# Kernel tuning notes

Hardware: AMD Instinct MI355X
Metric: run time of the kernel (lower is better)

Reference implementation:

```python
import jax, jax.numpy as jnp
import numpy as np

B, N, D = 2, 2048, 1024
H, DH = 16, 64
DI = 4096
EPS = 1e-5
NEG_SLOPE = 0.01  # F.leaky_relu default


def _ln(x, g, b):
    mu = jnp.mean(x, axis=-1, keepdims=True)
    var = jnp.mean((x - mu) ** 2, axis=-1, keepdims=True)
    return (x - mu) * jax.lax.rsqrt(var + EPS) * g + b


def setup_inputs() -> dict:
    key = jax.random.key(0)
    ks = jax.random.split(key, 10)
    s = 0.02
    return {
        "Z": jax.random.normal(ks[0], (B, N, D), jnp.float32),
        "new_mask": jax.random.normal(ks[1], (B, N, N), jnp.float32),
        "mask": jax.random.uniform(ks[2], (B, N, N), jnp.float32),
        "ln1_g": jnp.ones((D,), jnp.float32),
        "ln1_b": jnp.zeros((D,), jnp.float32),
        "qkv_w": jax.random.normal(ks[3], (3 * D, D), jnp.float32) * s,
        "qkv_b": jnp.zeros((3 * D,), jnp.float32),
        "o_w": jax.random.normal(ks[4], (D, H * DH), jnp.float32) * s,
        "ln2_g": jnp.ones((D,), jnp.float32),
        "ln2_b": jnp.zeros((D,), jnp.float32),
        "p1_w": jax.random.normal(ks[5], (DI, D), jnp.float32) * s,
        "p1_b": jnp.zeros((DI,), jnp.float32),
        "p2_w": jax.random.normal(ks[6], (D, DI), jnp.float32) * s,
        "p2_b": jnp.zeros((D,), jnp.float32),
    }


def reference(Z, new_mask, mask, ln1_g, ln1_b, qkv_w, qkv_b, o_w, ln2_g, ln2_b, p1_w, p1_b, p2_w, p2_b):
    inp = Z
    Zn = _ln(Z, ln1_g, ln1_b)
    qkv = (Zn @ qkv_w.T + qkv_b).reshape(B, N, H, 3 * DH)
    # torch chunk order in the source: V, Q, K
    V, Q, K = jnp.split(qkv, 3, axis=3)  # each [B,N,H,DH]
    # scores: einsum('bnij,bmij->binm') == [B,H,N,N]
    W = jnp.einsum("bnhd,bmhd->bhnm", Q, K) / np.sqrt(DH) + new_mask[:, None]
    A = jax.nn.softmax(W, axis=3) * mask[:, None]
    attn = jnp.einsum("bhnm,bmhd->bnhd", A, V).reshape(B, N, D)
    attn = jnp.where(attn >= 0, attn, NEG_SLOPE * attn) @ o_w.T  # leaky_relu then o_net (no bias)
    Z1 = attn + inp
    Zn2 = _ln(Z1, ln2_g, ln2_b)
    h = jax.nn.relu(Zn2 @ p1_w.T + p1_b)
    return h @ p2_w.T + p2_b + Z1
```

## Files before the change

### kernel.cpp

```cpp
#include <hip/hip_runtime.h>

typedef unsigned short u16;
typedef __attribute__((ext_vector_type(8))) short bf16x8;
typedef __attribute__((ext_vector_type(4))) float f32x4;

#define DEV static __device__ __forceinline__

DEV u16 f2bf(float f) {
    unsigned u = __float_as_uint(f);
    u += 0x7FFFu + ((u >> 16) & 1u);
    return (u16)(u >> 16);
}

typedef const __attribute__((address_space(1))) void* gas1_t;
typedef __attribute__((address_space(3))) void* gas3_t;

DEV void gl_lds16(const u16* g, u16* l) {
    __builtin_amdgcn_global_load_lds((gas1_t)g, (gas3_t)l, 16, 0, 0);
}

DEV int sw8(int row, int chunk) { return row * 64 + ((chunk ^ (row & 7)) << 3); }

__global__ void cast_bf16(const float* __restrict__ in, u16* __restrict__ out, int n4) {
    int i = blockIdx.x * blockDim.x + threadIdx.x;
    if (i < n4) {
        float4 v = ((const float4*)in)[i];
        ushort4 o;
        o.x = f2bf(v.x); o.y = f2bf(v.y); o.z = f2bf(v.z); o.w = f2bf(v.w);
        ((ushort4*)out)[i] = o;
    }
}

__global__ void cast_qkv(const float* __restrict__ in, u16* __restrict__ out) {
    int i = blockIdx.x * 256 + threadIdx.x;
    int orow = i >> 8, cc = i & 255;
    int region = orow >> 10, rem = orow & 1023, h = rem >> 6, t = rem & 63;
    int srow = h * 192 + region * 64 + t;
    float4 v = ((const float4*)in)[srow * 256 + cc];
    ushort4 o;
    o.x = f2bf(v.x); o.y = f2bf(v.y); o.z = f2bf(v.z); o.w = f2bf(v.w);
    ((ushort4*)out)[i] = o;
}

__global__ void permute_bias(const float* __restrict__ in, float* __restrict__ out) {
    int i = blockIdx.x * 256 + threadIdx.x;
    if (i < 3072) {
        int region = i >> 10, rem = i & 1023, h = rem >> 6, t = rem & 63;
        out[i] = in[h * 192 + region * 64 + t];
    }
}

__global__ void pack_mask(const float* __restrict__ nm, const float* __restrict__ pm,
                          unsigned* __restrict__ out, int n4) {
    int i = blockIdx.x * blockDim.x + threadIdx.x;
    if (i < n4) {
        float4 a = ((const float4*)nm)[i];
        float4 b = ((const float4*)pm)[i];
        uint4 o;
        o.x = ((unsigned)f2bf(b.x) << 16) | f2bf(a.x * 1.4426950f);
        o.y = ((unsigned)f2bf(b.y) << 16) | f2bf(a.y * 1.4426950f);
        o.z = ((unsigned)f2bf(b.z) << 16) | f2bf(a.z * 1.4426950f);
        o.w = ((unsigned)f2bf(b.w) << 16) | f2bf(a.w * 1.4426950f);
        ((uint4*)out)[i] = o;
    }
}

__global__ __launch_bounds__(256) void ln_bf16(const float* __restrict__ x,
                                               const float* __restrict__ gam,
                                               const float* __restrict__ bet,
                                               u16* __restrict__ y) {
    const int row = blockIdx.x;
    const int t = threadIdx.x;
    const float4 v = ((const float4*)(x + (size_t)row * 1024))[t];
    float s = v.x + v.y + v.z + v.w;
    float ss = v.x * v.x + v.y * v.y + v.z * v.z + v.w * v.w;
#pragma unroll
    for (int o = 1; o < 64; o <<= 1) {
        s += __shfl_xor(s, o);
        ss += __shfl_xor(ss, o);
    }
    __shared__ float rs[4], rss[4];
    const int wave = t >> 6, lane = t & 63;
    if (lane == 0) { rs[wave] = s; rss[wave] = ss; }
    __syncthreads();
    const float tot = rs[0] + rs[1] + rs[2] + rs[3];
    const float totss = rss[0] + rss[1] + rss[2] + rss[3];
    const float mu = tot * (1.0f / 1024.0f);
    const float var = totss * (1.0f / 1024.0f) - mu * mu;
    const float rstd = rsqrtf(var + 1e-5f);
    const float4 g4 = ((const float4*)gam)[t];
    const float4 b4 = ((const float4*)bet)[t];
    ushort4 o;
    o.x = f2bf((v.x - mu) * rstd * g4.x + b4.x);
    o.y = f2bf((v.y - mu) * rstd * g4.y + b4.y);
    o.z = f2bf((v.z - mu) * rstd * g4.z + b4.z);
    o.w = f2bf((v.w - mu) * rstd * g4.w + b4.w);
    ((ushort4*)(y + (size_t)row * 1024))[t] = o;
}

template <int EPI>
__global__ __launch_bounds__(256, 2) void gemm_bt(const u16* __restrict__ A,
                                                  const u16* __restrict__ Bt,
                                                  const float* __restrict__ bias,
                                                  const float* __restrict__ res,
                                                  void* __restrict__ out0,
                                                  void* __restrict__ out1,
                                                  void* __restrict__ out2,
                                                  int M, int N, int K) {
    __shared__ __align__(16) u16 As[128 * 32];
    __shared__ __align__(16) u16 Bs[128 * 32];
    const int tid = threadIdx.x;
    const int wave = tid >> 6, lane = tid & 63;
    const int lhi = lane >> 4, llo = lane & 15;
    const int bx = blockIdx.x, by = blockIdx.y;

    const int arow = wave * 32 + (lane >> 2);
    const int acol = (lane & 3) * 8;
    const u16* gA = A + (size_t)(by * 128 + arow) * K + acol;
    const u16* gB = Bt + (size_t)(bx * 128 + arow) * K + acol;
    u16* lA = As + wave * 1024 + lane * 8;
    u16* lB = Bs + wave * 1024 + lane * 8;

    const int wr = wave >> 1, wc = wave & 1;
    const f32x4 zero = {0.f, 0.f, 0.f, 0.f};
    f32x4 acc[4][4];
#pragma unroll
    for (int i = 0; i < 4; i++)
#pragma unroll
        for (int j = 0; j < 4; j++) acc[i][j] = zero;

    for (int k0 = 0; k0 < K; k0 += 32) {
        __syncthreads();
        gl_lds16(gA, lA);
        gl_lds16(gA + 16 * (size_t)K, lA + 512);
        gl_lds16(gB, lB);
        gl_lds16(gB + 16 * (size_t)K, lB + 512);
        gA += 32; gB += 32;
        __syncthreads();
        bf16x8 af[4], bfr[4];
#pragma unroll
        for (int i = 0; i < 4; i++)
            af[i] = *(const bf16x8*)(As + (wr * 64 + i * 16 + llo) * 32 + lhi * 8);
#pragma unroll
        for (int j = 0; j < 4; j++)
            bfr[j] = *(const bf16x8*)(Bs + (wc * 64 + j * 16 + llo) * 32 + lhi * 8);
#pragma unroll
        for (int i = 0; i < 4; i++)
#pragma unroll
            for (int j = 0; j < 4; j++)
                acc[i][j] = __builtin_amdgcn_mfma_f32_16x16x32_bf16(af[i], bfr[j], acc[i][j], 0, 0, 0);
    }

    const int rbase = by * 128 + wr * 64 + lhi * 4;
    const int cbase = bx * 128 + wc * 64 + llo;
#pragma unroll
    for (int i = 0; i < 4; i++) {
#pragma unroll
        for (int j = 0; j < 4; j++) {
#pragma unroll
            for (int r = 0; r < 4; r++) {
                const int row = rbase + i * 16 + r;
                const int col = cbase + j * 16;
                float v = acc[i][j][r];
                if (EPI == 0) {
                    v += bias[col];
                    const int region = col >> 10;
                    const int c = col & 1023;
                    const int b = row >> 11, n = row & 2047;
                    if (region == 0) {
                        ((float*)out0)[(size_t)row * 1024 + c] = v;
                    } else {
                        const int h = c >> 6, t = c & 63;
                        u16* dst = (region == 1) ? (u16*)out1 : (u16*)out2;
                        dst[(((size_t)(b * 16 + h)) * 2048 + n) * 64 + t] = f2bf(v);
                    }
                } else if (EPI == 1) {
                    ((float*)out0)[(size_t)row * N + col] = v + res[(size_t)row * N + col];
                } else if (EPI == 2) {
                    v += bias[col];
                    v = v > 0.f ? v : 0.f;
                    ((u16*)out0)[(size_t)row * N + col] = f2bf(v);
                } else {
                    v += bias[col] + res[(size_t)row * N + col];
                    ((float*)out0)[(size_t)row * N + col] = v;
                }
            }
        }
    }
}

__global__ __launch_bounds__(256) void vtrans(const float* __restrict__ Vsc,
                                              u16* __restrict__ Vt) {
    __shared__ u16 Ts[64 * 72];
    const int nt = blockIdx.x;
    const int bh = blockIdx.y;
    const int b = bh >> 4, h = bh & 15;
    const int t = threadIdx.x;
    const int n0 = nt * 64;
    const int nr = t >> 2;
    const int dq = (t & 3) * 16;
    const float* src = Vsc + ((size_t)(b * 2048 + n0 + nr)) * 1024 + h * 64 + dq;
    float4 v0 = ((const float4*)src)[0];
    float4 v1 = ((const float4*)src)[1];
    float4 v2 = ((const float4*)src)[2];
    float4 v3 = ((const float4*)src)[3];
    u16* c0 = Ts + nr;
    c0[(dq + 0) * 72]  = f2bf(v0.x); c0[(dq + 1) * 72]  = f2bf(v0.y);
    c0[(dq + 2) * 72]  = f2bf(v0.z); c0[(dq + 3) * 72]  = f2bf(v0.w);
    c0[(dq + 4) * 72]  = f2bf(v1.x); c0[(dq + 5) * 72]  = f2bf(v1.y);
    c0[(dq + 6) * 72]  = f2bf(v1.z); c0[(dq + 7) * 72]  = f2bf(v1.w);
    c0[(dq + 8) * 72]  = f2bf(v2.x); c0[(dq + 9) * 72]  = f2bf(v2.y);
    c0[(dq + 10) * 72] = f2bf(v2.z); c0[(dq + 11) * 72] = f2bf(v2.w);
    c0[(dq + 12) * 72] = f2bf(v3.x); c0[(dq + 13) * 72] = f2bf(v3.y);
    c0[(dq + 14) * 72] = f2bf(v3.z); c0[(dq + 15) * 72] = f2bf(v3.w);
    __syncthreads();
    const int d = t >> 2, n8 = (t & 3) * 16;
    bf16x8 o0 = *(const bf16x8*)(Ts + d * 72 + n8);
    bf16x8 o1 = *(const bf16x8*)(Ts + d * 72 + n8 + 8);
    u16* dst = Vt + ((size_t)bh * 64 + d) * 2048 + n0 + n8;
    *(bf16x8*)dst = o0;
    *(bf16x8*)(dst + 8) = o1;
}

__global__ __launch_bounds__(256, 2) void attn_fused2(const u16* __restrict__ Qg,
                                                      const u16* __restrict__ Kg,
                                                      const u16* __restrict__ Vt,
                                                      const unsigned* __restrict__ Mp,
                                                      u16* __restrict__ attnL) {
    __shared__ __align__(16) u16 Qs[128 * 64];
    __shared__ __align__(16) u16 Ks[64 * 64];
    __shared__ __align__(16) u16 Vs[64 * 64];
    __shared__ __align__(16) u16 Ps[128 * 64];
    const int tid = threadIdx.x, wave = tid >> 6, lane = tid & 63;
    const int lhi = lane >> 4, llo = lane & 15;
    const int id = blockIdx.x;
    const int hh = id >> 5, bq = id & 31;
    const int b = bq >> 4, qt = bq & 15;
    const int bh = b * 16 + hh;
    const int q0 = qt * 128;
    const int l3 = lane >> 3, l7 = lane & 7;
    const int swcol = (l7 ^ (l3 & 7)) * 8;

#pragma unroll
    for (int s = 0; s < 4; s++) {
        const int row = wave * 32 + s * 8 + l3;
        gl_lds16(Qg + ((size_t)bh * 2048 + q0 + row) * 64 + swcol,
                 Qs + wave * 2048 + s * 512 + lane * 8);
    }

    const unsigned* Mpb = Mp + (size_t)b * 2048 * 2048;
    int midx[2][4];
#pragma unroll
    for (int i = 0; i < 2; i++)
#pragma unroll
        for (int r = 0; r < 4; r++)
            midx[i][r] = (q0 + wave * 32 + i * 16 + lhi * 4 + r) * 2048 + llo;

    const f32x4 zero = {0.f, 0.f, 0.f, 0.f};
    f32x4 accO[2][4];
    float lsum[2][4];
#pragma unroll
    for (int i = 0; i < 2; i++)
#pragma unroll
        for (int j = 0; j < 4; j++) accO[i][j] = zero;
#pragma unroll
    for (int i = 0; i < 2; i++)
#pragma unroll
        for (int r = 0; r < 4; r++) lsum[i][r] = 0.f;

    const float CS = 0.125f * 1.4426950f;

    for (int m0 = 0; m0 < 2048; m0 += 64) {
        __syncthreads();
#pragma unroll
        for (int s = 0; s < 2; s++) {
            const int row = wave * 16 + s * 8 + l3;
            gl_lds16(Kg + ((size_t)bh * 2048 + m0 + row) * 64 + swcol,
                     Ks + wave * 1024 + s * 512 + lane * 8);
            gl_lds16(Vt + ((size_t)bh * 64 + row) * 2048 + m0 + swcol,
                     Vs + wave * 1024 + s * 512 + lane * 8);
        }
        unsigned mv[2][4][4];
#pragma unroll
        for (int i = 0; i < 2; i++)
#pragma unroll
            for (int r = 0; r < 4; r++)
#pragma unroll
                for (int j = 0; j < 4; j++)
                    mv[i][r][j] = Mpb[midx[i][r] + m0 + j * 16];
        __syncthreads();

        f32x4 sacc[2][4];
#pragma unroll
        for (int i = 0; i < 2; i++)
#pragma unroll
            for (int j = 0; j < 4; j++) sacc[i][j] = zero;
#pragma unroll
        for (int kk = 0; kk < 2; kk++) {
            bf16x8 aq[2];
#pragma unroll
            for (int i = 0; i < 2; i++)
                aq[i] = *(const bf16x8*)(Qs + sw8(wave * 32 + i * 16 + llo, kk * 4 + lhi));
#pragma unroll
            for (int j = 0; j < 4; j++) {
                const bf16x8 bk = *(const bf16x8*)(Ks + sw8(j * 16 + llo, kk * 4 + lhi));
                sacc[0][j] = __builtin_amdgcn_mfma_f32_16x16x32_bf16(aq[0], bk, sacc[0][j], 0, 0, 0);
                sacc[1][j] = __builtin_amdgcn_mfma_f32_16x16x32_bf16(aq[1], bk, sacc[1][j], 0, 0, 0);
            }
        }

#pragma unroll
        for (int i = 0; i < 2; i++)
#pragma unroll
            for (int j = 0; j < 4; j++)
#pragma unroll
                for (int r = 0; r < 4; r++) {
                    const unsigned u = mv[i][r][j];
                    const float nm = __uint_as_float(u << 16);
                    const float pm = __uint_as_float(u & 0xFFFF0000u);
                    const float e = exp2f(fmaf(sacc[i][j][r], CS, nm));
                    lsum[i][r] += e;
                    const float p = e * pm;
                    const u16 pb = (u16)((__float_as_uint(p) + 0x8000u) >> 16);
                    const int q_rel = wave * 32 + i * 16 + lhi * 4 + r;
                    const int ch = (j * 2 + (llo >> 3)) ^ (q_rel & 7);
                    Ps[q_rel * 64 + ch * 8 + (llo & 7)] = pb;
                }

#pragma unroll
        for (int kk = 0; kk < 2; kk++) {
            bf16x8 ap[2];
#pragma unroll
            for (int i = 0; i < 2; i++)
                ap[i] = *(const bf16x8*)(Ps + sw8(wave * 32 + i * 16 + llo, kk * 4 + lhi));
#pragma unroll
            for (int jd = 0; jd < 4; jd++) {
                const bf16x8 bv = *(const bf16x8*)(Vs + sw8(jd * 16 + llo, kk * 4 + lhi));
                accO[0][jd] = __builtin_amdgcn_mfma_f32_16x16x32_bf16(ap[0], bv, accO[0][jd], 0, 0, 0);
                accO[1][jd] = __builtin_amdgcn_mfma_f32_16x16x32_bf16(ap[1], bv, accO[1][jd], 0, 0, 0);
            }
        }
    }

#pragma unroll
    for (int i = 0; i < 2; i++)
#pragma unroll
        for (int r = 0; r < 4; r++) {
#pragma unroll
            for (int o = 1; o < 16; o <<= 1) lsum[i][r] += __shfl_xor(lsum[i][r], o);
            lsum[i][r] = 1.0f / lsum[i][r];
        }
#pragma unroll
    for (int i = 0; i < 2; i++)
#pragma unroll
        for (int jd = 0; jd < 4; jd++)
#pragma unroll
            for (int r = 0; r < 4; r++) {
                float v = accO[i][jd][r] * lsum[i][r];
                v = v >= 0.f ? v : 0.01f * v;
                const int q = q0 + wave * 32 + i * 16 + lhi * 4 + r;
                attnL[((size_t)b * 2048 + q) * 1024 + hh * 64 + jd * 16 + llo] = f2bf(v);
            }
}

extern "C" void kernel_launch(void* const* d_in, const int* in_sizes, int n_in,
                              void* d_out, int out_size, void* d_ws, size_t ws_size,
                              hipStream_t stream) {
    const float* Z     = (const float*)d_in[0];
    const float* nmask = (const float*)d_in[1];
    const float* pmask = (const float*)d_in[2];
    const float* ln1_g = (const float*)d_in[3];
    const float* ln1_b = (const float*)d_in[4];
    const float* qkv_w = (const float*)d_in[5];
    const float* qkv_b = (const float*)d_in[6];
    const float* o_w   = (const float*)d_in[7];
    const float* ln2_g = (const float*)d_in[8];
    const float* ln2_b = (const float*)d_in[9];
    const float* p1_w  = (const float*)d_in[10];
    const float* p1_b  = (const float*)d_in[11];
    const float* p2_w  = (const float*)d_in[12];
    const float* p2_b  = (const float*)d_in[13];
    float* out = (float*)d_out;

    char* w = (char*)d_ws;
    auto take = [&](size_t bytes) -> char* {
        char* p = w;
        w += (bytes + 255) & ~(size_t)255;
        return p;
    };
    u16* qkvW   = (u16*)take((size_t)3072 * 1024 * 2);
    u16* oW     = (u16*)take((size_t)1024 * 1024 * 2);
    u16* p1W    = (u16*)take((size_t)4096 * 1024 * 2);
    u16* p2W    = (u16*)take((size_t)1024 * 4096 * 2);
    u16* Zn     = (u16*)take((size_t)4096 * 1024 * 2);
    u16* Qb     = (u16*)take((size_t)32 * 2048 * 64 * 2);
    u16* Kb     = (u16*)take((size_t)32 * 2048 * 64 * 2);
    u16* Vt     = (u16*)take((size_t)32 * 64 * 2048 * 2);
    u16* attnL  = (u16*)take((size_t)4096 * 1024 * 2);
    float* Z1   = (float*)take((size_t)4096 * 1024 * 4);
    u16* hbuf   = (u16*)take((size_t)4096 * 4096 * 2);
    unsigned* Mp = (unsigned*)take((size_t)2 * 2048 * 2048 * 4);
    float* pbias = (float*)take((size_t)3072 * 4);
    float* Vsc   = (float*)hbuf;

    cast_qkv<<<dim3(3072), 256, 0, stream>>>(qkv_w, qkvW);
    permute_bias<<<dim3(12), 256, 0, stream>>>(qkv_b, pbias);
    cast_bf16<<<dim3(1024), 256, 0, stream>>>(o_w, oW, 1024 * 1024 / 4);
    cast_bf16<<<dim3(4096), 256, 0, stream>>>(p1_w, p1W, 4096 * 1024 / 4);
    cast_bf16<<<dim3(4096), 256, 0, stream>>>(p2_w, p2W, 1024 * 4096 / 4);
    pack_mask<<<dim3(8192), 256, 0, stream>>>(nmask, pmask, Mp, 2 * 2048 * 2048 / 4);

    ln_bf16<<<dim3(4096), 256, 0, stream>>>(Z, ln1_g, ln1_b, Zn);
    gemm_bt<0><<<dim3(24, 32), 256, 0, stream>>>(Zn, qkvW, pbias, nullptr, Vsc, Qb, Kb, 4096, 3072, 1024);
    vtrans<<<dim3(32, 32), 256, 0, stream>>>(Vsc, Vt);
    attn_fused2<<<dim3(512), 256, 0, stream>>>(Qb, Kb, Vt, Mp, attnL);
    gemm_bt<1><<<dim3(8, 32), 256, 0, stream>>>(attnL, oW, nullptr, Z, Z1, nullptr, nullptr, 4096, 1024, 1024);
    ln_bf16<<<dim3(4096), 256, 0, stream>>>(Z1, ln2_g, ln2_b, Zn);
    gemm_bt<2><<<dim3(32, 32), 256, 0, stream>>>(Zn, p1W, p1_b, nullptr, hbuf, nullptr, nullptr, 4096, 4096, 1024);
    gemm_bt<3><<<dim3(8, 32), 256, 0, stream>>>(hbuf, p2W, p2_b, Z1, out, nullptr, nullptr, 4096, 1024, 4096);
}
```

Before: 476.3 us.

## Split-K narrow GEMMs with fused combine kernels and halve attention query tile

The two N=1024 GEMMs (o-proj and FFN down) now run with split-K=2 over a z grid dimension. They write fp32 partials into the reused mask buffer, and new combine kernels reduce the partials, with residual and bias folded in. LN2 is fused into the o-proj combine. The attention kernel now uses 64-row query tiles with 4 blocks per CU instead of 128-row tiles at 2 per CU, doubling the block count and using a padded P buffer. The aim is better occupancy and CU fill for grids that were too small (256 blocks, 512 blocks), at the cost of extra partial-sum traffic and less Q reuse per K/V tile.

```diff
diff --git a/kernel.cpp b/kernel.cpp
--- a/kernel.cpp
+++ b/kernel.cpp
@@ -98,26 +98,84 @@
     ((ushort4*)(y + (size_t)row * 1024))[t] = o;
 }
 
+__global__ __launch_bounds__(256) void ln2_comb(const float* __restrict__ p0,
+                                                const float* __restrict__ p1,
+                                                const float* __restrict__ Z,
+                                                const float* __restrict__ gam,
+                                                const float* __restrict__ bet,
+                                                float* __restrict__ Z1,
+                                                u16* __restrict__ y) {
+    const int row = blockIdx.x;
+    const int t = threadIdx.x;
+    const float4 a = ((const float4*)(p0 + (size_t)row * 1024))[t];
+    const float4 c = ((const float4*)(p1 + (size_t)row * 1024))[t];
+    const float4 z = ((const float4*)(Z + (size_t)row * 1024))[t];
+    float4 v;
+    v.x = a.x + c.x + z.x; v.y = a.y + c.y + z.y;
+    v.z = a.z + c.z + z.z; v.w = a.w + c.w + z.w;
+    ((float4*)(Z1 + (size_t)row * 1024))[t] = v;
+    float s = v.x + v.y + v.z + v.w;
+    float ss = v.x * v.x + v.y * v.y + v.z * v.z + v.w * v.w;
+#pragma unroll
+    for (int o = 1; o < 64; o <<= 1) {
+        s += __shfl_xor(s, o);
+        ss += __shfl_xor(ss, o);
+    }
+    __shared__ float rs[4], rss[4];
+    const int wave = t >> 6, lane = t & 63;
+    if (lane == 0) { rs[wave] = s; rss[wave] = ss; }
+    __syncthreads();
+    const float tot = rs[0] + rs[1] + rs[2] + rs[3];
+    const float totss = rss[0] + rss[1] + rss[2] + rss[3];
+    const float mu = tot * (1.0f / 1024.0f);
+    const float var = totss * (1.0f / 1024.0f) - mu * mu;
+    const float rstd = rsqrtf(var + 1e-5f);
+    const float4 g4 = ((const float4*)gam)[t];
+    const float4 b4 = ((const float4*)bet)[t];
+    ushort4 o;
+    o.x = f2bf((v.x - mu) * rstd * g4.x + b4.x);
+    o.y = f2bf((v.y - mu) * rstd * g4.y + b4.y);
+    o.z = f2bf((v.z - mu) * rstd * g4.z + b4.z);
+    o.w = f2bf((v.w - mu) * rstd * g4.w + b4.w);
+    ((ushort4*)(y + (size_t)row * 1024))[t] = o;
+}
+
+__global__ __launch_bounds__(256) void out_comb(const float* __restrict__ p0,
+                                                const float* __restrict__ p1,
+                                                const float* __restrict__ bias,
+                                                const float* __restrict__ Z1,
+                                                float* __restrict__ out) {
+    int i = blockIdx.x * 256 + threadIdx.x;
+    float4 a = ((const float4*)p0)[i];
+    float4 c = ((const float4*)p1)[i];
+    float4 z = ((const float4*)Z1)[i];
+    float4 b = ((const float4*)bias)[i & 255];
+    float4 o;
+    o.x = a.x + c.x + z.x + b.x; o.y = a.y + c.y + z.y + b.y;
+    o.z = a.z + c.z + z.z + b.z; o.w = a.w + c.w + z.w + b.w;
+    ((float4*)out)[i] = o;
+}
+
 template <int EPI>
 __global__ __launch_bounds__(256, 2) void gemm_bt(const u16* __restrict__ A,
                                                   const u16* __restrict__ Bt,
                                                   const float* __restrict__ bias,
-                                                  const float* __restrict__ res,
                                                   void* __restrict__ out0,
                                                   void* __restrict__ out1,
                                                   void* __restrict__ out2,
-                                                  int M, int N, int K) {
+                                                  int M, int N, int K, int ldk) {
     __shared__ __align__(16) u16 As[128 * 32];
     __shared__ __align__(16) u16 Bs[128 * 32];
     const int tid = threadIdx.x;
     const int wave = tid >> 6, lane = tid & 63;
     const int lhi = lane >> 4, llo = lane & 15;
     const int bx = blockIdx.x, by = blockIdx.y;
+    const int kz = blockIdx.z * K;
 
     const int arow = wave * 32 + (lane >> 2);
     const int acol = (lane & 3) * 8;
-    const u16* gA = A + (size_t)(by * 128 + arow) * K + acol;
-    const u16* gB = Bt + (size_t)(bx * 128 + arow) * K + acol;
+    const u16* gA = A + (size_t)(by * 128 + arow) * ldk + kz + acol;
+    const u16* gB = Bt + (size_t)(bx * 128 + arow) * ldk + kz + acol;
     u16* lA = As + wave * 1024 + lane * 8;
     u16* lB = Bs + wave * 1024 + lane * 8;
 
@@ -132,9 +190,9 @@
     for (int k0 = 0; k0 < K; k0 += 32) {
         __syncthreads();
         gl_lds16(gA, lA);
-        gl_lds16(gA + 16 * (size_t)K, lA + 512);
+        gl_lds16(gA + 16 * (size_t)ldk, lA + 512);
         gl_lds16(gB, lB);
-        gl_lds16(gB + 16 * (size_t)K, lB + 512);
+        gl_lds16(gB + 16 * (size_t)ldk, lB + 512);
         gA += 32; gB += 32;
         __syncthreads();
         bf16x8 af[4], bfr[4];
@@ -153,6 +211,7 @@
 
     const int rbase = by * 128 + wr * 64 + lhi * 4;
     const int cbase = bx * 128 + wc * 64 + llo;
+    float* pout = (EPI == 4) ? ((float*)out0 + (size_t)blockIdx.z * M * N) : (float*)out0;
 #pragma unroll
     for (int i = 0; i < 4; i++) {
 #pragma unroll
@@ -162,7 +221,7 @@
                 const int row = rbase + i * 16 + r;
                 const int col = cbase + j * 16;
                 float v = acc[i][j][r];
-                if (EPI == 0) {
+                if constexpr (EPI == 0) {
                     v += bias[col];
                     const int region = col >> 10;
                     const int c = col & 1023;
@@ -174,15 +233,12 @@
                         u16* dst = (region == 1) ? (u16*)out1 : (u16*)out2;
                         dst[(((size_t)(b * 16 + h)) * 2048 + n) * 64 + t] = f2bf(v);
                     }
-                } else if (EPI == 1) {
-                    ((float*)out0)[(size_t)row * N + col] = v + res[(size_t)row * N + col];
-                } else if (EPI == 2) {
+                } else if constexpr (EPI == 2) {
                     v += bias[col];
                     v = v > 0.f ? v : 0.f;
                     ((u16*)out0)[(size_t)row * N + col] = f2bf(v);
                 } else {
-                    v += bias[col] + res[(size_t)row * N + col];
-                    ((float*)out0)[(size_t)row * N + col] = v;
+                    pout[(size_t)row * N + col] = v;
                 }
             }
         }
@@ -222,53 +278,48 @@
     *(bf16x8*)(dst + 8) = o1;
 }
 
-__global__ __launch_bounds__(256, 2) void attn_fused2(const u16* __restrict__ Qg,
+__global__ __launch_bounds__(256, 4) void attn_fused4(const u16* __restrict__ Qg,
                                                       const u16* __restrict__ Kg,
                                                       const u16* __restrict__ Vt,
                                                       const unsigned* __restrict__ Mp,
                                                       u16* __restrict__ attnL) {
-    __shared__ __align__(16) u16 Qs[128 * 64];
+    __shared__ __align__(16) u16 Qs[64 * 64];
     __shared__ __align__(16) u16 Ks[64 * 64];
     __shared__ __align__(16) u16 Vs[64 * 64];
-    __shared__ __align__(16) u16 Ps[128 * 64];
+    __shared__ __align__(16) u16 Ps[64 * 72];
     const int tid = threadIdx.x, wave = tid >> 6, lane = tid & 63;
     const int lhi = lane >> 4, llo = lane & 15;
     const int id = blockIdx.x;
-    const int hh = id >> 5, bq = id & 31;
-    const int b = bq >> 4, qt = bq & 15;
+    const int hh = id >> 6, rem = id & 63;
+    const int b = rem >> 5, qt = rem & 31;
     const int bh = b * 16 + hh;
-    const int q0 = qt * 128;
+    const int q0 = qt * 64;
     const int l3 = lane >> 3, l7 = lane & 7;
     const int swcol = (l7 ^ (l3 & 7)) * 8;
 
 #pragma unroll
-    for (int s = 0; s < 4; s++) {
-        const int row = wave * 32 + s * 8 + l3;
+    for (int s = 0; s < 2; s++) {
+        const int row = wave * 16 + s * 8 + l3;
         gl_lds16(Qg + ((size_t)bh * 2048 + q0 + row) * 64 + swcol,
-                 Qs + wave * 2048 + s * 512 + lane * 8);
+                 Qs + wave * 1024 + s * 512 + lane * 8);
     }
 
     const unsigned* Mpb = Mp + (size_t)b * 2048 * 2048;
-    int midx[2][4];
-#pragma unroll
-    for (int i = 0; i < 2; i++)
-#pragma unroll
-        for (int r = 0; r < 4; r++)
-            midx[i][r] = (q0 + wave * 32 + i * 16 + lhi * 4 + r) * 2048 + llo;
+    int midx[4];
+#pragma unroll
+    for (int r = 0; r < 4; r++)
+        midx[r] = (q0 + wave * 16 + lhi * 4 + r) * 2048 + llo;
 
     const f32x4 zero = {0.f, 0.f, 0.f, 0.f};
-    f32x4 accO[2][4];
-    float lsum[2][4];
-#pragma unroll
-    for (int i = 0; i < 2; i++)
-#pragma unroll
-        for (int j = 0; j < 4; j++) accO[i][j] = zero;
-#pragma unroll
-    for (int i = 0; i < 2; i++)
-#pragma unroll
-        for (int r = 0; r < 4; r++) lsum[i][r] = 0.f;
+    f32x4 accO[4];
+    float lsum[4];
+#pragma unroll
+    for (int j = 0; j < 4; j++) accO[j] = zero;
+#pragma unroll
+    for (int r = 0; r < 4; r++) lsum[r] = 0.f;
 
     const float CS = 0.125f * 1.4426950f;
+    const int pb0 = (wave * 16 + lhi * 4) * 72 + llo;
 
     for (int m0 = 0; m0 < 2048; m0 += 64) {
         __syncthreads();
@@ -280,87 +331,65 @@
             gl_lds16(Vt + ((size_t)bh * 64 + row) * 2048 + m0 + swcol,
                      Vs + wave * 1024 + s * 512 + lane * 8);
         }
-        unsigned mv[2][4][4];
-#pragma unroll
-        for (int i = 0; i < 2; i++)
-#pragma unroll
-            for (int r = 0; r < 4; r++)
-#pragma unroll
-                for (int j = 0; j < 4; j++)
-                    mv[i][r][j] = Mpb[midx[i][r] + m0 + j * 16];
+        unsigned mv[4][4];
+#pragma unroll
+        for (int r = 0; r < 4; r++)
+#pragma unroll
+            for (int j = 0; j < 4; j++) mv[r][j] = Mpb[midx[r] + m0 + j * 16];
         __syncthreads();
 
-        f32x4 sacc[2][4];
-#pragma unroll
-        for (int i = 0; i < 2; i++)
-#pragma unroll
-            for (int j = 0; j < 4; j++) sacc[i][j] = zero;
+        f32x4 sacc[4];
+#pragma unroll
+        for (int j = 0; j < 4; j++) sacc[j] = zero;
 #pragma unroll
         for (int kk = 0; kk < 2; kk++) {
-            bf16x8 aq[2];
-#pragma unroll
-            for (int i = 0; i < 2; i++)
-                aq[i] = *(const bf16x8*)(Qs + sw8(wave * 32 + i * 16 + llo, kk * 4 + lhi));
+            const bf16x8 aq = *(const bf16x8*)(Qs + sw8(wave * 16 + llo, kk * 4 + lhi));
 #pragma unroll
             for (int j = 0; j < 4; j++) {
                 const bf16x8 bk = *(const bf16x8*)(Ks + sw8(j * 16 + llo, kk * 4 + lhi));
-                sacc[0][j] = __builtin_amdgcn_mfma_f32_16x16x32_bf16(aq[0], bk, sacc[0][j], 0, 0, 0);
-                sacc[1][j] = __builtin_amdgcn_mfma_f32_16x16x32_bf16(aq[1], bk, sacc[1][j], 0, 0, 0);
+                sacc[j] = __builtin_amdgcn_mfma_f32_16x16x32_bf16(aq, bk, sacc[j], 0, 0, 0);
             }
         }
 
 #pragma unroll
-        for (int i = 0; i < 2; i++)
-#pragma unroll
-            for (int j = 0; j < 4; j++)
-#pragma unroll
-                for (int r = 0; r < 4; r++) {
-                    const unsigned u = mv[i][r][j];
-                    const float nm = __uint_as_float(u << 16);
-                    const float pm = __uint_as_float(u & 0xFFFF0000u);
-                    const float e = exp2f(fmaf(sacc[i][j][r], CS, nm));
-                    lsum[i][r] += e;
-                    const float p = e * pm;
-                    const u16 pb = (u16)((__float_as_uint(p) + 0x8000u) >> 16);
-                    const int q_rel = wave * 32 + i * 16 + lhi * 4 + r;
-                    const int ch = (j * 2 + (llo >> 3)) ^ (q_rel & 7);
-                    Ps[q_rel * 64 + ch * 8 + (llo & 7)] = pb;
-                }
+        for (int j = 0; j < 4; j++)
+#pragma unroll
+            for (int r = 0; r < 4; r++) {
+                const unsigned u = mv[r][j];
+                const float nm = __uint_as_float(u << 16);
+                const float pm = __uint_as_float(u & 0xFFFF0000u);
+                const float e = exp2f(fmaf(sacc[j][r], CS, nm));
+                lsum[r] += e;
+                const float p = e * pm;
+                Ps[pb0 + r * 72 + j * 16] = (u16)((__float_as_uint(p) + 0x8000u) >> 16);
+            }
 
 #pragma unroll
         for (int kk = 0; kk < 2; kk++) {
-            bf16x8 ap[2];
-#pragma unroll
-            for (int i = 0; i < 2; i++)
-                ap[i] = *(const bf16x8*)(Ps + sw8(wave * 32 + i * 16 + llo, kk * 4 + lhi));
+            const bf16x8 ap = *(const bf16x8*)(Ps + (wave * 16 + llo) * 72 + kk * 32 + lhi * 8);
 #pragma unroll
             for (int jd = 0; jd < 4; jd++) {
                 const bf16x8 bv = *(const bf16x8*)(Vs + sw8(jd * 16 + llo, kk * 4 + lhi));
-                accO[0][jd] = __builtin_amdgcn_mfma_f32_16x16x32_bf16(ap[0], bv, accO[0][jd], 0, 0, 0);
-                accO[1][jd] = __builtin_amdgcn_mfma_f32_16x16x32_bf16(ap[1], bv, accO[1][jd], 0, 0, 0);
+                accO[jd] = __builtin_amdgcn_mfma_f32_16x16x32_bf16(ap, bv, accO[jd], 0, 0, 0);
             }
         }
     }
 
 #pragma unroll
-    for (int i = 0; i < 2; i++)
+    for (int r = 0; r < 4; r++) {
+#pragma unroll
+        for (int o = 1; o < 16; o <<= 1) lsum[r] += __shfl_xor(lsum[r], o);
+        lsum[r] = 1.0f / lsum[r];
+    }
+#pragma unroll
+    for (int jd = 0; jd < 4; jd++)
 #pragma unroll
         for (int r = 0; r < 4; r++) {
-#pragma unroll
-            for (int o = 1; o < 16; o <<= 1) lsum[i][r] += __shfl_xor(lsum[i][r], o);
-            lsum[i][r] = 1.0f / lsum[i][r];
+            float v = accO[jd][r] * lsum[r];
+            v = v >= 0.f ? v : 0.01f * v;
+            const int q = q0 + wave * 16 + lhi * 4 + r;
+            attnL[((size_t)b * 2048 + q) * 1024 + hh * 64 + jd * 16 + llo] = f2bf(v);
         }
-#pragma unroll
-    for (int i = 0; i < 2; i++)
-#pragma unroll
-        for (int jd = 0; jd < 4; jd++)
-#pragma unroll
-            for (int r = 0; r < 4; r++) {
-                float v = accO[i][jd][r] * lsum[i][r];
-                v = v >= 0.f ? v : 0.01f * v;
-                const int q = q0 + wave * 32 + i * 16 + lhi * 4 + r;
-                attnL[((size_t)b * 2048 + q) * 1024 + hh * 64 + jd * 16 + llo] = f2bf(v);
-            }
 }
 
 extern "C" void kernel_launch(void* const* d_in, const int* in_sizes, int n_in,
@@ -402,6 +431,8 @@
     unsigned* Mp = (unsigned*)take((size_t)2 * 2048 * 2048 * 4);
     float* pbias = (float*)take((size_t)3072 * 4);
     float* Vsc   = (float*)hbuf;
+    float* part  = (float*)Mp;
+    float* part1 = part + (size_t)4096 * 1024;
 
     cast_qkv<<<dim3(3072), 256, 0, stream>>>(qkv_w, qkvW);
     permute_bias<<<dim3(12), 256, 0, stream>>>(qkv_b, pbias);
@@ -411,11 +442,12 @@
     pack_mask<<<dim3(8192), 256, 0, stream>>>(nmask, pmask, Mp, 2 * 2048 * 2048 / 4);
 
     ln_bf16<<<dim3(4096), 256, 0, stream>>>(Z, ln1_g, ln1_b, Zn);
-    gemm_bt<0><<<dim3(24, 32), 256, 0, stream>>>(Zn, qkvW, pbias, nullptr, Vsc, Qb, Kb, 4096, 3072, 1024);
+    gemm_bt<0><<<dim3(24, 32), 256, 0, stream>>>(Zn, qkvW, pbias, Vsc, Qb, Kb, 4096, 3072, 1024, 1024);
     vtrans<<<dim3(32, 32), 256, 0, stream>>>(Vsc, Vt);
-    attn_fused2<<<dim3(512), 256, 0, stream>>>(Qb, Kb, Vt, Mp, attnL);
-    gemm_bt<1><<<dim3(8, 32), 256, 0, stream>>>(attnL, oW, nullptr, Z, Z1, nullptr, nullptr, 4096, 1024, 1024);
-    ln_bf16<<<dim3(4096), 256, 0, stream>>>(Z1, ln2_g, ln2_b, Zn);
-    gemm_bt<2><<<dim3(32, 32), 256, 0, stream>>>(Zn, p1W, p1_b, nullptr, hbuf, nullptr, nullptr, 4096, 4096, 1024);
-    gemm_bt<3><<<dim3(8, 32), 256, 0, stream>>>(hbuf, p2W, p2_b, Z1, out, nullptr, nullptr, 4096, 1024, 4096);
-}
+    attn_fused4<<<dim3(1024), 256, 0, stream>>>(Qb, Kb, Vt, Mp, attnL);
+    gemm_bt<4><<<dim3(8, 32, 2), 256, 0, stream>>>(attnL, oW, nullptr, part, nullptr, nullptr, 4096, 1024, 512, 1024);
+    ln2_comb<<<dim3(4096), 256, 0, stream>>>(part, part1, Z, ln2_g, ln2_b, Z1, Zn);
+    gemm_bt<2><<<dim3(32, 32), 256, 0, stream>>>(Zn, p1W, p1_b, hbuf, nullptr, nullptr, 4096, 4096, 1024, 1024);
+    gemm_bt<4><<<dim3(8, 32, 2), 256, 0, stream>>>(hbuf, p2W, nullptr, part, nullptr, nullptr, 4096, 1024, 2048, 4096);
+    out_comb<<<dim3(4096), 256, 0, stream>>>(part, part1, p2_b, Z1, out);
+}
```

New measurement: 445.5 us. 6.5% less time.
